# Optimization experiments

Measured on AMD Instinct MI355X. Metric: run time of the kernel, lower is better.

## Reference

```python
import jax, jax.numpy as jnp
import numpy as np

N_NODES = 100000
N_EDGES = 3200000
N_GRAPHS = 256
DIMS = [11, 200, 200, 200, 200, 200]  # acfg_init_dims + cfg_filters
CONCAT = sum(DIMS[1:])  # 1000


def setup_inputs() -> dict:
    key = jax.random.key(0)
    ks = jax.random.split(key, 32)
    d = {}
    d["x"] = jax.random.normal(ks[0], (N_NODES, DIMS[0]), jnp.float32)
    d["edge_index"] = jax.random.randint(ks[1], (2, N_EDGES), 0, N_NODES)
    d["batch"] = jnp.sort(jax.random.randint(ks[2], (N_NODES,), 0, N_GRAPHS))
    ki = 3
    # SAGEConv params: lin_l (neighbors, with bias) + lin_r (root, no bias)
    for i in range(5):
        fi, fo = DIMS[i], DIMS[i + 1]
        s = 1.0 / np.sqrt(fi)
        d[f"Wl{i+1}"] = jax.random.uniform(ks[ki], (fo, fi), jnp.float32, -s, s); ki += 1
        d[f"bl{i+1}"] = jnp.zeros((fo,), jnp.float32)
        d[f"Wr{i+1}"] = jax.random.uniform(ks[ki], (fo, fi), jnp.float32, -s, s); ki += 1
    # projection head 1000 -> 500 -> 250 -> 1
    for j, (fi, fo) in enumerate([(CONCAT, CONCAT // 2), (CONCAT // 2, CONCAT // 4), (CONCAT // 4, 1)]):
        s = 1.0 / np.sqrt(fi)
        d[f"pw{j+1}"] = jax.random.uniform(ks[ki], (fo, fi), jnp.float32, -s, s); ki += 1
        d[f"pb{j+1}"] = jnp.zeros((fo,), jnp.float32)
    return d


def reference(x, edge_index, batch,
              Wl1, bl1, Wr1, Wl2, bl2, Wr2, Wl3, bl3, Wr3,
              Wl4, bl4, Wr4, Wl5, bl5, Wr5,
              pw1, pb1, pw2, pb2, pw3, pb3):
    src, dst = edge_index[0], edge_index[1]
    # in-degree for mean aggregation (computed once, reused by all layers)
    deg = jax.ops.segment_sum(jnp.ones((src.shape[0],), x.dtype), dst, N_NODES)
    inv_deg = (1.0 / jnp.maximum(deg, 1.0))[:, None]

    def sage(h, Wl, bl, Wr):
        agg = jax.ops.segment_sum(h[src], dst, N_NODES) * inv_deg  # mean of neighbor feats
        return agg @ Wl.T + bl + h @ Wr.T

    layers = [(Wl1, bl1, Wr1), (Wl2, bl2, Wr2), (Wl3, bl3, Wr3), (Wl4, bl4, Wr4), (Wl5, bl5, Wr5)]
    h = x
    outs = []
    for Wl, bl, Wr in layers:
        h = jax.nn.relu(sage(h, Wl, bl, Wr))
        outs.append(h)
    hc = jnp.concatenate(outs, axis=1)  # [N, 1000]

    # global_mean_pool over graph ids
    cnt = jax.ops.segment_sum(jnp.ones((x.shape[0],), x.dtype), batch, N_GRAPHS)
    g = jax.ops.segment_sum(hc, batch, N_GRAPHS) / jnp.maximum(cnt, 1.0)[:, None]

    # dropout is identity in eval mode (functional.dropout with training=False)
    g = g @ pw1.T + pb1
    g = g @ pw2.T + pb2
    g = g @ pw3.T + pb3  # [num_graphs, 1]
    return jax.nn.sigmoid(g).squeeze(1)
```

## Files before the change

### kernel.cpp

```cpp
#include <hip/hip_runtime.h>
#include <math.h>

typedef __attribute__((ext_vector_type(4))) float floatx4;
typedef __attribute__((ext_vector_type(2))) float floatx2;

#define ROWP 256
#define R4   16
#define NT 14
#define NTC 13
#define KS 7
#define PACK_BYTES (NT*KS*64*8)
#define PACK1_BYTES (NT*64*8)
#define STAGE_BYTES (NTC*KS*64*8)
#define BSHIFT 6
#define EPB 8192
#define MAXBUCK 1600
#define PT_STRIDE 208

__device__ __forceinline__ unsigned short f2bf(float f){
    union { float f; unsigned u; } v; v.f = f;
    unsigned r = v.u + 0x7FFF + ((v.u >> 16) & 1);
    return (unsigned short)(r >> 16);
}
__device__ __forceinline__ unsigned pk4_fp8(float a, float b, float c, float d){
    int w = __builtin_amdgcn_cvt_pk_fp8_f32(a, b, 0, false);
    w = __builtin_amdgcn_cvt_pk_fp8_f32(c, d, w, true);
    return (unsigned)w;
}
__device__ __forceinline__ unsigned char b1_fp8(float a){
    int w = __builtin_amdgcn_cvt_pk_fp8_f32(a, a, 0, false);
    return (unsigned char)(w & 0xFF);
}


__global__ __launch_bounds__(256) void k_bin_hist(
    const int* __restrict__ dst, int* __restrict__ hist, int E, int nbuck)
{
    __shared__ int lh[MAXBUCK];
    for (int i = threadIdx.x; i < nbuck; i += 256) lh[i] = 0;
    __syncthreads();
    int base = blockIdx.x * EPB;
    #pragma unroll
    for (int k = 0; k < EPB / 256; ++k){
        int e = base + k * 256 + threadIdx.x;
        if (e < E) atomicAdd(&lh[dst[e] >> BSHIFT], 1);
    }
    __syncthreads();
    for (int i = threadIdx.x; i < nbuck; i += 256)
        hist[(size_t)blockIdx.x * nbuck + i] = lh[i];
}

__global__ __launch_bounds__(256) void k_col_scan(
    int* __restrict__ hist, int* __restrict__ T, int nblk, int nbuck)
{
    __shared__ int part[4][64];
    int w = threadIdx.x >> 6, l = threadIdx.x & 63;
    int b = blockIdx.x * 64 + l;
    int chunk = (nblk + 3) >> 2;
    int j0 = w * chunk, j1 = j0 + chunk; if (j1 > nblk) j1 = nblk;
    int s = 0;
    if (b < nbuck)
        for (int j = j0; j < j1; ++j) s += hist[(size_t)j * nbuck + b];
    part[w][l] = s;
    __syncthreads();
    if (b < nbuck){
        int run = 0;
        for (int w2 = 0; w2 < w; ++w2) run += part[w2][l];
        for (int j = j0; j < j1; ++j){
            int v = hist[(size_t)j * nbuck + b];
            hist[(size_t)j * nbuck + b] = run;
            run += v;
        }
        if (w == 3) T[b] = part[0][l] + part[1][l] + part[2][l] + part[3][l];
    }
}

__global__ __launch_bounds__(256) void k_scan_t(
    const int* __restrict__ T, int* __restrict__ tbase, int nbuck,
    const int* __restrict__ batch, int* __restrict__ gstart, int N, int NG)
{
    __shared__ int ts[256];
    int t = threadIdx.x;
    int v[8]; int s = 0;
    int base = t * 8;
    #pragma unroll
    for (int k = 0; k < 8; ++k){
        int idx = base + k;
        v[k] = (idx < nbuck) ? T[idx] : 0;
        s += v[k];
    }
    ts[t] = s; __syncthreads();
    #pragma unroll
    for (int off = 1; off < 256; off <<= 1){
        int p = (t >= off) ? ts[t - off] : 0;
        __syncthreads();
        ts[t] += p;
        __syncthreads();
    }
    int run = ts[t] - s;
    #pragma unroll
    for (int k = 0; k < 8; ++k){
        int idx = base + k;
        if (idx < nbuck) tbase[idx] = run;
        run += v[k];
    }
    if (t == 255) tbase[nbuck] = ts[255];

    for (int g = t; g <= NG; g += 256){
        int lo = 0, hi = N;
        while (lo < hi){
            int mid = (lo + hi) >> 1;
            if (batch[mid] < g) lo = mid + 1; else hi = mid;
        }
        gstart[g] = lo;
    }
}

__global__ __launch_bounds__(256) void k_bin_scatter(
    const int* __restrict__ src, const int* __restrict__ dst,
    const int* __restrict__ off, const int* __restrict__ tbase,
    unsigned* __restrict__ pairs, int E, int nbuck)
{
    __shared__ int lbase[MAXBUCK];
    __shared__ int lc[MAXBUCK];
    for (int i = threadIdx.x; i < nbuck; i += 256){
        lbase[i] = off[(size_t)blockIdx.x * nbuck + i] + tbase[i];
        lc[i] = 0;
    }
    __syncthreads();
    int base = blockIdx.x * EPB;
    #pragma unroll
    for (int k = 0; k < EPB / 256; ++k){
        int e = base + k * 256 + threadIdx.x;
        if (e < E){
            int d = dst[e];
            int b = d >> BSHIFT;
            int r = atomicAdd(&lc[b], 1);
            pairs[lbase[b] + r] = ((unsigned)(d & 63) << 26) | (unsigned)src[e];
        }
    }
}

__global__ __launch_bounds__(256) void k_bucket_deg(
    const unsigned* __restrict__ pairs, const int* __restrict__ tbase,
    int* __restrict__ deg, float* __restrict__ inv_deg, int N)
{
    __shared__ int ld[64];
    int b = blockIdx.x;
    if (threadIdx.x < 64) ld[threadIdx.x] = 0;
    __syncthreads();
    int pb = tbase[b], pe = tbase[b + 1];
    for (int e = pb + threadIdx.x; e < pe; e += 256)
        atomicAdd(&ld[pairs[e] >> 26], 1);
    __syncthreads();
    if (threadIdx.x < 64){
        int node = (b << BSHIFT) + threadIdx.x;
        if (node < N){
            int d = ld[threadIdx.x];
            deg[node] = d;
            inv_deg[node] = 1.0f / fmaxf((float)d, 1.0f);
        }
    }
}

__global__ __launch_bounds__(256) void k_place(
    const unsigned* __restrict__ pairs, const int* __restrict__ tbase,
    const int* __restrict__ row_ptr, int* __restrict__ srcs, int N)
{
    __shared__ int lrp[64];
    __shared__ int lcur[64];
    int b = blockIdx.x;
    if (threadIdx.x < 64){
        int node = (b << BSHIFT) + threadIdx.x;
        lrp[threadIdx.x] = (node < N) ? row_ptr[node] : 0;
        lcur[threadIdx.x] = 0;
    }
    __syncthreads();
    int pb = tbase[b], pe = tbase[b + 1];
    for (int e = pb + threadIdx.x; e < pe; e += 256){
        unsigned pr = pairs[e];
        int li = pr >> 26;
        int r = atomicAdd(&lcur[li], 1);
        srcs[lrp[li] + r] = (int)(pr & 0x03FFFFFFu);
    }
}


__global__ void k_scan_sums(const int* __restrict__ deg, int* __restrict__ csum, int N){
    __shared__ int sd[256];
    int base = blockIdx.x * 1024;
    int s = 0;
    for (int i = threadIdx.x; i < 1024; i += 256){
        int idx = base + i;
        s += (idx < N) ? deg[idx] : 0;
    }
    sd[threadIdx.x] = s; __syncthreads();
    for (int off = 128; off > 0; off >>= 1){
        if (threadIdx.x < off) sd[threadIdx.x] += sd[threadIdx.x + off];
        __syncthreads();
    }
    if (threadIdx.x == 0) csum[blockIdx.x] = sd[0];
}

__global__ void k_scan_apply(const int* __restrict__ deg, const int* __restrict__ csum,
                             int* __restrict__ row_ptr, int N, int E, int nchunks){
    __shared__ int ts[256];
    __shared__ int base_s;
    int partial = 0;
    for (int j = threadIdx.x; j < nchunks; j += 256)
        if (j < (int)blockIdx.x) partial += csum[j];
    ts[threadIdx.x] = partial; __syncthreads();
    for (int off = 128; off > 0; off >>= 1){
        if (threadIdx.x < off) ts[threadIdx.x] += ts[threadIdx.x + off];
        __syncthreads();
    }
    if (threadIdx.x == 0) base_s = ts[0];
    __syncthreads();
    int blk_base = base_s;
    __syncthreads();

    int base = blockIdx.x * 1024 + threadIdx.x * 4;
    int v[4]; int s = 0;
    #pragma unroll
    for (int j = 0; j < 4; ++j){
        int idx = base + j;
        v[j] = (idx < N) ? deg[idx] : 0;
        s += v[j];
    }
    ts[threadIdx.x] = s; __syncthreads();
    #pragma unroll
    for (int off = 1; off < 256; off <<= 1){
        int t = (threadIdx.x >= off) ? ts[threadIdx.x - off] : 0;
        __syncthreads();
        ts[threadIdx.x] += t;
        __syncthreads();
    }
    int excl = ts[threadIdx.x] - s + blk_base;
    #pragma unroll
    for (int j = 0; j < 4; ++j){
        int idx = base + j;
        if (idx < N) row_ptr[idx] = excl;
        excl += v[j];
    }
    if (blockIdx.x == 0 && threadIdx.x == 0) row_ptr[N] = E;
}


__global__ void k_pack_w(const float* W0, const float* W1, const float* W2, const float* W3,
                         const float* W4, const float* W5, const float* W6, const float* W7,
                         unsigned char* __restrict__ out){
    const float* Ws[8] = {W0,W1,W2,W3,W4,W5,W6,W7};
    const float* W = Ws[blockIdx.z];
    int lane = threadIdx.x;
    int n  = blockIdx.x * 16 + (lane & 15);
    int k0 = blockIdx.y * 32 + (lane >> 4) * 8;
    float f[8];
    #pragma unroll
    for (int j = 0; j < 8; ++j){
        int k = k0 + j;
        f[j] = (n < 200 && k < 200) ? W[n * 200 + k] : 0.f;
    }
    uint2 u;
    u.x = pk4_fp8(f[0], f[1], f[2], f[3]);
    u.y = pk4_fp8(f[4], f[5], f[6], f[7]);
    size_t off = ((((size_t)blockIdx.z * NT + blockIdx.x) * KS + blockIdx.y) * 64 + lane) * 8;
    *reinterpret_cast<uint2*>(out + off) = u;
}

__global__ __launch_bounds__(256) void k_pack_misc(
    const float* __restrict__ x, unsigned short* __restrict__ xp,
    unsigned char* __restrict__ xa,
    const float* __restrict__ Wl1, const float* __restrict__ Wr1,
    unsigned char* __restrict__ w1pack,
    const float* b0, const float* b1, const float* b2, const float* b3, const float* b4,
    float* __restrict__ biasp, int N, int xblk)
{
    int bid = blockIdx.x;
    if (bid < xblk){
        int i = bid * 256 + threadIdx.x;
        int node = i >> 4, c = i & 15;
        if (node < N){
            float f = (c < 11) ? x[(size_t)node * 11 + c] : 0.f;
            xp[i] = f2bf(f);
            xa[(size_t)node * 32 + 16 + c] = b1_fp8(f);
        }
        return;
    }
    int j = bid - xblk;
    if (j < NT){
        if (threadIdx.x >= 64) return;
        int lane = threadIdx.x;
        int n  = j * 16 + (lane & 15);
        int k0 = (lane >> 4) * 8;
        float f[8];
        #pragma unroll
        for (int jj = 0; jj < 8; ++jj){
            int k = k0 + jj;
            float v = 0.f;
            if (n < 200){
                if (k < 11)                 v = Wl1[n * 11 + k];
                else if (k >= 16 && k < 27) v = Wr1[n * 11 + (k - 16)];
            }
            f[jj] = v;
        }
        uint2 u;
        u.x = pk4_fp8(f[0], f[1], f[2], f[3]);
        u.y = pk4_fp8(f[4], f[5], f[6], f[7]);
        size_t off = ((size_t)j * 64 + lane) * 8;
        *reinterpret_cast<uint2*>(w1pack + off) = u;
        return;
    }
    int l = j - NT;
    const float* bs[5] = {b0,b1,b2,b3,b4};
    int c = threadIdx.x;
    if (c < ROWP) biasp[l * ROWP + c] = (c < 200) ? bs[l][c] : 0.f;
}


__global__ __launch_bounds__(256) void k_agg11(
    const unsigned short* __restrict__ xp, const int* __restrict__ row_ptr,
    const int* __restrict__ srcs, const float* __restrict__ inv_deg,
    unsigned char* __restrict__ xa, int N)
{
    int half = threadIdx.x >> 5;
    int node = blockIdx.x * 8 + half;
    int l = threadIdx.x & 31;
    if (node >= N) return;
    int beg = row_ptr[node], end = row_ptr[node + 1];

    float acc[12];
    #pragma unroll
    for (int i = 0; i < 12; ++i) acc[i] = 0.f;

    const uint4* x4 = reinterpret_cast<const uint4*>(xp);
    const uint2* x2 = reinterpret_cast<const uint2*>(xp);
    for (int e = beg + l; e < end; e += 32){
        int sn = srcs[e];
        uint4 a = x4[(size_t)sn * 2];
        uint2 b = x2[(size_t)sn * 4 + 2];
        union { unsigned u; float f; } c;
        c.u = a.x << 16;         acc[0] += c.f;
        c.u = a.x & 0xffff0000u; acc[1] += c.f;
        c.u = a.y << 16;         acc[2] += c.f;
        c.u = a.y & 0xffff0000u; acc[3] += c.f;
        c.u = a.z << 16;         acc[4] += c.f;
        c.u = a.z & 0xffff0000u; acc[5] += c.f;
        c.u = a.w << 16;         acc[6] += c.f;
        c.u = a.w & 0xffff0000u; acc[7] += c.f;
        c.u = b.x << 16;         acc[8] += c.f;
        c.u = b.x & 0xffff0000u; acc[9] += c.f;
        c.u = b.y << 16;         acc[10] += c.f;
        c.u = b.y & 0xffff0000u; acc[11] += c.f;
    }

    #pragma unroll
    for (int i = 0; i < 11; ++i){
        acc[i] += __shfl_xor(acc[i], 1, 64);
        acc[i] += __shfl_xor(acc[i], 2, 64);
        acc[i] += __shfl_xor(acc[i], 4, 64);
        acc[i] += __shfl_xor(acc[i], 8, 64);
        acc[i] += __shfl_xor(acc[i], 16, 64);
    }

    if (l == 0){
        float id = inv_deg[node];
        float v[12];
        #pragma unroll
        for (int i = 0; i < 11; ++i) v[i] = acc[i] * id;
        v[11] = 0.f;
        uint4 o;
        o.x = pk4_fp8(v[0], v[1], v[2], v[3]);
        o.y = pk4_fp8(v[4], v[5], v[6], v[7]);
        o.z = pk4_fp8(v[8], v[9], v[10], v[11]);
        o.w = 0u;
        *reinterpret_cast<uint4*>(xa + (size_t)node * 32) = o;
    }
}


__device__ __forceinline__ void accum_fp8v(floatx2* a, uint4 u){
    a[0] += __builtin_amdgcn_cvt_pk_f32_fp8((int)u.x, false);
    a[1] += __builtin_amdgcn_cvt_pk_f32_fp8((int)u.x, true );
    a[2] += __builtin_amdgcn_cvt_pk_f32_fp8((int)u.y, false);
    a[3] += __builtin_amdgcn_cvt_pk_f32_fp8((int)u.y, true );
    a[4] += __builtin_amdgcn_cvt_pk_f32_fp8((int)u.z, false);
    a[5] += __builtin_amdgcn_cvt_pk_f32_fp8((int)u.z, true );
    a[6] += __builtin_amdgcn_cvt_pk_f32_fp8((int)u.w, false);
    a[7] += __builtin_amdgcn_cvt_pk_f32_fp8((int)u.w, true );
}

__global__ __launch_bounds__(256) void k_agg200(
    const unsigned char* __restrict__ h8, const int* __restrict__ row_ptr,
    const int* __restrict__ srcs, const float* __restrict__ inv_deg,
    unsigned char* __restrict__ agg, int N)
{
    int node = blockIdx.x * 4 + (threadIdx.x >> 6);
    int lane = threadIdx.x & 63;
    if (node >= N) return;
    int g = lane >> 4;
    int l = lane & 15;
    int beg = row_ptr[node], end = row_ptr[node + 1];
    int nb = end - beg;

    floatx2 acc[8];
    #pragma unroll
    for (int i = 0; i < 8; ++i) acc[i] = (floatx2){0.f, 0.f};

    const uint4* h4 = reinterpret_cast<const uint4*>(h8);

    for (int t = 0; t < nb; t += 64){
        int cnt = nb - t; if (cnt > 64) cnt = 64;
        int eidx = t + lane;
        int si = srcs[beg + (eidx < nb ? eidx : nb - 1)];
        int jmax = (cnt - g + 3) >> 2;

        int j = 0;
        for (; j + 4 <= jmax; j += 4){
            int b0 = g + 4 * j;
            int s0 = __shfl(si, b0,      64);
            int s1 = __shfl(si, b0 + 4,  64);
            int s2 = __shfl(si, b0 + 8,  64);
            int s3 = __shfl(si, b0 + 12, 64);
            uint4 u0 = h4[(size_t)s0 * R4 + l];
            uint4 u1 = h4[(size_t)s1 * R4 + l];
            uint4 u2 = h4[(size_t)s2 * R4 + l];
            uint4 u3 = h4[(size_t)s3 * R4 + l];
            accum_fp8v(acc, u0);
            accum_fp8v(acc, u1);
            accum_fp8v(acc, u2);
            accum_fp8v(acc, u3);
        }
        for (; j < jmax; ++j){
            int s0 = __shfl(si, g + 4 * j, 64);
            uint4 u0 = h4[(size_t)s0 * R4 + l];
            accum_fp8v(acc, u0);
        }
    }

    float af[16];
    #pragma unroll
    for (int i = 0; i < 8; ++i){ af[2*i] = acc[i][0]; af[2*i+1] = acc[i][1]; }
    #pragma unroll
    for (int i = 0; i < 16; ++i){
        af[i] += __shfl_xor(af[i], 32, 64);
        af[i] += __shfl_xor(af[i], 16, 64);
    }

    if (g == 0){
        float id = inv_deg[node];
        uint4 o;
        o.x = pk4_fp8(af[0] * id,  af[1] * id,  af[2] * id,  af[3] * id);
        o.y = pk4_fp8(af[4] * id,  af[5] * id,  af[6] * id,  af[7] * id);
        o.z = pk4_fp8(af[8] * id,  af[9] * id,  af[10] * id, af[11] * id);
        o.w = pk4_fp8(af[12] * id, af[13] * id, af[14] * id, af[15] * id);
        *reinterpret_cast<uint4*>(agg + (size_t)node * ROWP + l * 16) = o;
    }
}


__global__ __launch_bounds__(256) void k_layer1_mfma(
    const unsigned char* __restrict__ xa, const unsigned char* __restrict__ W1p,
    const float* __restrict__ biasp, const int* __restrict__ batch,
    float* __restrict__ gsum, unsigned char* __restrict__ outp, int M)
{
    __shared__ __align__(16) unsigned char ptile[64 * PT_STRIDE];
    __shared__ int lb[64];
    const int wave = threadIdx.x >> 6;
    const int lane = threadIdx.x & 63;
    const int n = lane & 15;
    const int q = lane >> 4;
    const int r0 = blockIdx.x * 64;
    const int nrows = (M - r0 < 64) ? (M - r0) : 64;
    int row = r0 + wave * 16 + n;
    int rowc = row < M ? row : (M - 1);

    if (threadIdx.x < 64 && threadIdx.x < nrows) lb[threadIdx.x] = batch[r0 + threadIdx.x];

    long a = *reinterpret_cast<const long*>(xa + (size_t)rowc * 32 + q * 8);

    floatx4 acc[NTC];
    #pragma unroll
    for (int nt = 0; nt < NTC; ++nt){
        long b = *reinterpret_cast<const long*>(W1p + ((size_t)nt * 64 + lane) * 8);
        acc[nt] = __builtin_amdgcn_mfma_f32_16x16x32_fp8_fp8(a, b, (floatx4){0.f,0.f,0.f,0.f}, 0, 0, 0);
    }

    {
        int lr0 = wave * 16 + q * 4;
        #pragma unroll
        for (int nt = 0; nt < NTC; ++nt){
            float bsv = biasp[nt * 16 + n];
            #pragma unroll
            for (int r = 0; r < 4; ++r){
                float v = fmaxf(acc[nt][r] + bsv, 0.f);
                ptile[(lr0 + r) * PT_STRIDE + nt * 16 + n] = b1_fp8(v);
            }
        }
    }
    __syncthreads();

    {
        const uint4* s4 = reinterpret_cast<const uint4*>(ptile);
        int tot = nrows * 13;
        for (int i = threadIdx.x; i < tot; i += 256){
            int r = i / 13, c = i - r * 13;
            *reinterpret_cast<uint4*>(outp + (size_t)(r0 + r) * ROWP + c * 16) = s4[i];
        }
    }

    if (threadIdx.x < 50){
        int t = threadIdx.x;
        const unsigned* pd = reinterpret_cast<const unsigned*>(ptile);
        float s0 = 0.f, s1 = 0.f, s2 = 0.f, s3 = 0.f;
        int cur = lb[0];
        for (int r = 0; r < nrows; ++r){
            int gg = lb[r];
            if (gg != cur){
                float* gp = &gsum[(size_t)cur * 1000 + t * 4];
                atomicAdd(gp + 0, s0); atomicAdd(gp + 1, s1);
                atomicAdd(gp + 2, s2); atomicAdd(gp + 3, s3);
                s0 = s1 = s2 = s3 = 0.f;
                cur = gg;
            }
            unsigned u = pd[r * 52 + t];
            floatx2 lo = __builtin_amdgcn_cvt_pk_f32_fp8((int)u, false);
            floatx2 hi = __builtin_amdgcn_cvt_pk_f32_fp8((int)u, true);
            s0 += lo[0]; s1 += lo[1]; s2 += hi[0]; s3 += hi[1];
        }
        float* gp = &gsum[(size_t)cur * 1000 + t * 4];
        atomicAdd(gp + 0, s0); atomicAdd(gp + 1, s1);
        atomicAdd(gp + 2, s2); atomicAdd(gp + 3, s3);
    }
}

__global__ __launch_bounds__(256) void k_sage_mfma(
    const unsigned char* __restrict__ Aagg, const unsigned char* __restrict__ Ah,
    const unsigned char* __restrict__ Wlp, const unsigned char* __restrict__ Wrp,
    const float* __restrict__ biasp, const int* __restrict__ batch,
    float* __restrict__ gsum, int col_off,
    unsigned char* __restrict__ outp, int M)
{
    __shared__ __align__(16) unsigned char lw[STAGE_BYTES];
    __shared__ int lb[64];
    const int wave = threadIdx.x >> 6;
    const int lane = threadIdx.x & 63;
    const int n = lane & 15;
    const int q = lane >> 4;
    const int r0 = blockIdx.x * 64;
    const int nrows = (M - r0 < 64) ? (M - r0) : 64;
    int row = r0 + wave * 16 + n;
    int rowc = row < M ? row : (M - 1);

    if (threadIdx.x < 64 && threadIdx.x < nrows) lb[threadIdx.x] = batch[r0 + threadIdx.x];

    floatx4 acc[NTC];
    #pragma unroll
    for (int nt = 0; nt < NTC; ++nt) acc[nt] = (floatx4){0.f, 0.f, 0.f, 0.f};

    const unsigned char* Wp[2] = {Wlp, Wrp};
    const unsigned char* Ap[2] = {Aagg, Ah};

    #pragma unroll
    for (int phase = 0; phase < 2; ++phase){
        if (phase) __syncthreads();

        const unsigned char* arow = Ap[phase] + (size_t)rowc * ROWP + q * 8;
        long a[KS];
        #pragma unroll
        for (int ks = 0; ks < 6; ++ks)
            a[ks] = *reinterpret_cast<const long*>(arow + ks * 32);
        a[6] = (q < 2) ? *reinterpret_cast<const long*>(arow + 192) : 0L;

        {
            const uint4* src4 = reinterpret_cast<const uint4*>(Wp[phase]);
            uint4* dst4 = reinterpret_cast<uint4*>(lw);
            for (int i = threadIdx.x; i < STAGE_BYTES / 16; i += 256)
                dst4[i] = src4[i];
        }
        __syncthreads();

        #pragma unroll
        for (int ks = 0; ks < KS; ++ks){
            #pragma unroll
            for (int nt = 0; nt < NTC; ++nt){
                long b = *reinterpret_cast<const long*>(&lw[((nt * KS + ks) * 64 + lane) * 8]);
                acc[nt] = __builtin_amdgcn_mfma_f32_16x16x32_fp8_fp8(a[ks], b, acc[nt], 0, 0, 0);
            }
        }
    }
    __syncthreads();

    unsigned char* ptile = lw;
    {
        int lr0 = wave * 16 + q * 4;
        #pragma unroll
        for (int nt = 0; nt < NTC; ++nt){
            float bsv = biasp[nt * 16 + n];
            #pragma unroll
            for (int r = 0; r < 4; ++r){
                float v = fmaxf(acc[nt][r] + bsv, 0.f);
                ptile[(lr0 + r) * PT_STRIDE + nt * 16 + n] = b1_fp8(v);
            }
        }
    }
    __syncthreads();

    {
        const uint4* s4 = reinterpret_cast<const uint4*>(ptile);
        int tot = nrows * 13;
        for (int i = threadIdx.x; i < tot; i += 256){
            int r = i / 13, c = i - r * 13;
            *reinterpret_cast<uint4*>(outp + (size_t)(r0 + r) * ROWP + c * 16) = s4[i];
        }
    }

    if (threadIdx.x < 50){
        int t = threadIdx.x;
        const unsigned* pd = reinterpret_cast<const unsigned*>(ptile);
        float s0 = 0.f, s1 = 0.f, s2 = 0.f, s3 = 0.f;
        int cur = lb[0];
        for (int r = 0; r < nrows; ++r){
            int gg = lb[r];
            if (gg != cur){
                float* gp = &gsum[(size_t)cur * 1000 + col_off + t * 4];
                atomicAdd(gp + 0, s0); atomicAdd(gp + 1, s1);
                atomicAdd(gp + 2, s2); atomicAdd(gp + 3, s3);
                s0 = s1 = s2 = s3 = 0.f;
                cur = gg;
            }
            unsigned u = pd[r * 52 + t];
            floatx2 lo = __builtin_amdgcn_cvt_pk_f32_fp8((int)u, false);
            floatx2 hi = __builtin_amdgcn_cvt_pk_f32_fp8((int)u, true);
            s0 += lo[0]; s1 += lo[1]; s2 += hi[0]; s3 += hi[1];
        }
        float* gp = &gsum[(size_t)cur * 1000 + col_off + t * 4];
        atomicAdd(gp + 0, s0); atomicAdd(gp + 1, s1);
        atomicAdd(gp + 2, s2); atomicAdd(gp + 3, s3);
    }
}


__global__ __launch_bounds__(256) void k_mlp_first(
    const float* __restrict__ gsum, const int* __restrict__ gstart,
    const float* __restrict__ W, const float* __restrict__ b,
    float* __restrict__ outp)
{
    __shared__ __align__(16) float row[1000];
    int g = blockIdx.x;
    int cnt = gstart[g+1] - gstart[g];
    float inv = 1.0f / fmaxf((float)cnt, 1.0f);
    for (int i = threadIdx.x; i < 1000; i += 256)
        row[i] = gsum[(size_t)g * 1000 + i] * inv;
    __syncthreads();
    for (int c = threadIdx.x; c < 500; c += 256){
        const float4* w4 = reinterpret_cast<const float4*>(W + (size_t)c * 1000);
        const float4* r4 = reinterpret_cast<const float4*>(row);
        float s = b[c];
        for (int k = 0; k < 250; ++k){
            float4 wv = w4[k]; float4 rv = r4[k];
            s = fmaf(wv.x, rv.x, s);
            s = fmaf(wv.y, rv.y, s);
            s = fmaf(wv.z, rv.z, s);
            s = fmaf(wv.w, rv.w, s);
        }
        outp[(size_t)g * 500 + c] = s;
    }
}

__global__ __launch_bounds__(256) void k_mlp23(
    const float* __restrict__ t1, const float* __restrict__ W2,
    const float* __restrict__ b2, const float* __restrict__ W3,
    const float* __restrict__ b3, float* __restrict__ outp)
{
    __shared__ __align__(16) float row[500];
    __shared__ float red[256];
    int g = blockIdx.x;
    for (int i = threadIdx.x; i < 500; i += 256) row[i] = t1[(size_t)g * 500 + i];
    __syncthreads();
    float prod = 0.f;
    int c = threadIdx.x;
    if (c < 250){
        const float4* w4 = reinterpret_cast<const float4*>(W2 + (size_t)c * 500);
        const float4* r4 = reinterpret_cast<const float4*>(row);
        float s = b2[c];
        for (int k = 0; k < 125; ++k){
            float4 wv = w4[k]; float4 rv = r4[k];
            s = fmaf(wv.x, rv.x, s);
            s = fmaf(wv.y, rv.y, s);
            s = fmaf(wv.z, rv.z, s);
            s = fmaf(wv.w, rv.w, s);
        }
        prod = s * W3[c];
    }
    red[threadIdx.x] = prod;
    __syncthreads();
    for (int off = 128; off > 0; off >>= 1){
        if (threadIdx.x < off) red[threadIdx.x] += red[threadIdx.x + off];
        __syncthreads();
    }
    if (threadIdx.x == 0)
        outp[g] = 1.0f / (1.0f + expf(-(red[0] + b3[0])));
}


extern "C" void kernel_launch(void* const* d_in, const int* in_sizes, int n_in,
                              void* d_out, int out_size, void* d_ws, size_t ws_size,
                              hipStream_t stream)
{
    const float* x    = (const float*)d_in[0];
    const int*   ei   = (const int*)d_in[1];
    const int*   batch= (const int*)d_in[2];
    const float* Wl[5]; const float* bl[5]; const float* Wr[5];
    for (int i = 0; i < 5; ++i){
        Wl[i] = (const float*)d_in[3 + 3*i];
        bl[i] = (const float*)d_in[4 + 3*i];
        Wr[i] = (const float*)d_in[5 + 3*i];
    }
    const float* pw1 = (const float*)d_in[18]; const float* pb1 = (const float*)d_in[19];
    const float* pw2 = (const float*)d_in[20]; const float* pb2 = (const float*)d_in[21];
    const float* pw3 = (const float*)d_in[22]; const float* pb3 = (const float*)d_in[23];
    float* out = (float*)d_out;

    const int N  = in_sizes[2];
    const int E  = in_sizes[1] / 2;
    const int NG = out_size;
    const int* esrc = ei;
    const int* edst = ei + E;
    const int nbuck = (N + 63) >> BSHIFT;
    const int nblk  = (E + EPB - 1) / EPB;

    char* p = (char*)d_ws;
    auto carve = [&](size_t bytes)->void* {
        void* r = (void*)p;
        p += (bytes + 255) & ~(size_t)255;
        return r;
    };
    int*   deg     = (int*)  carve((size_t)N * 4);
    int*   row_ptr = (int*)  carve(((size_t)N + 1) * 4);
    int*   csum    = (int*)  carve(4096);
    int*   hist    = (int*)  carve((size_t)nblk * nbuck * 4);
    int*   Tb      = (int*)  carve((size_t)nbuck * 4);
    int*   tbase   = (int*)  carve(((size_t)nbuck + 1) * 4);
    float* invdeg  = (float*)carve((size_t)N * 4);
    int*   gstart  = (int*)  carve(((size_t)NG + 1) * 4);
    int*   srcs    = (int*)  carve((size_t)E * 4);
    unsigned* pairs = (unsigned*)carve((size_t)E * 4);
    unsigned short* xp    = (unsigned short*)carve((size_t)N * 16 * 2);
    unsigned char*  xa    = (unsigned char*) carve((size_t)N * 32);
    unsigned char*  agg8  = (unsigned char*) carve((size_t)N * ROWP);
    unsigned char*  h8A   = (unsigned char*) carve((size_t)N * ROWP);
    unsigned char*  h8B   = (unsigned char*) carve((size_t)N * ROWP);
    unsigned char*  wpack = (unsigned char*) carve((size_t)8 * PACK_BYTES);
    unsigned char*  w1pack= (unsigned char*) carve((size_t)PACK1_BYTES);
    float* biasp   = (float*)carve((size_t)5 * ROWP * 4);
    float* gsum    = (float*)carve((size_t)NG * 1000 * 4);
    float* t1      = (float*)carve((size_t)NG * 500 * 4);

    hipMemsetAsync(gsum, 0, (size_t)NG * 1000 * 4, stream);
    hipMemsetAsync(h8A, 0, (size_t)N * ROWP, stream);
    hipMemsetAsync(h8B, 0, (size_t)N * ROWP, stream);

    int xblk = (N * 16 + 255) / 256;
    k_pack_w<<<dim3(NT, KS, 8), 64, 0, stream>>>(
        Wl[1], Wr[1], Wl[2], Wr[2], Wl[3], Wr[3], Wl[4], Wr[4], wpack);
    k_pack_misc<<<xblk + NT + 5, 256, 0, stream>>>(
        x, xp, xa, Wl[0], Wr[0], w1pack,
        bl[0], bl[1], bl[2], bl[3], bl[4], biasp, N, xblk);

    k_bin_hist<<<nblk, 256, 0, stream>>>(edst, hist, E, nbuck);
    k_col_scan<<<(nbuck + 63) / 64, 256, 0, stream>>>(hist, Tb, nblk, nbuck);
    k_scan_t<<<1, 256, 0, stream>>>(Tb, tbase, nbuck, batch, gstart, N, NG);
    k_bin_scatter<<<nblk, 256, 0, stream>>>(esrc, edst, hist, tbase, pairs, E, nbuck);
    k_bucket_deg<<<nbuck, 256, 0, stream>>>(pairs, tbase, deg, invdeg, N);
    int nchunks = (N + 1023) / 1024;
    k_scan_sums<<<nchunks, 256, 0, stream>>>(deg, csum, N);
    k_scan_apply<<<nchunks, 256, 0, stream>>>(deg, csum, row_ptr, N, E, nchunks);
    k_place<<<nbuck, 256, 0, stream>>>(pairs, tbase, row_ptr, srcs, N);

    int gb = (N + 63) / 64;
    k_agg11<<<(N + 7) / 8, 256, 0, stream>>>(xp, row_ptr, srcs, invdeg, xa, N);
    k_layer1_mfma<<<gb, 256, 0, stream>>>(xa, w1pack, biasp, batch, gsum, h8A, N);

    unsigned char* hc = h8A; unsigned char* hn = h8B;
    int ab = (N + 3) / 4;
    for (int L = 1; L < 5; ++L){
        k_agg200<<<ab, 256, 0, stream>>>(hc, row_ptr, srcs, invdeg, agg8, N);
        const unsigned char* Wlp = wpack + (size_t)((L-1)*2 + 0) * PACK_BYTES;
        const unsigned char* Wrp = wpack + (size_t)((L-1)*2 + 1) * PACK_BYTES;
        k_sage_mfma<<<gb, 256, 0, stream>>>(agg8, hc, Wlp, Wrp,
                                            biasp + L * ROWP, batch, gsum, 200 * L,
                                            hn, N);
        unsigned char* t = hc; hc = hn; hn = t;
    }

    k_mlp_first<<<NG, 256, 0, stream>>>(gsum, gstart, pw1, pb1, t1);
    k_mlp23<<<NG, 256, 0, stream>>>(t1, pw2, pb2, pw3, pb3, out);
}
```

Before: 1.082 ms.

## Fuse bucket degree, row-pointer scan and placement into one kernel

Replaces the four-kernel CSR build (bucket degree, two-pass global scan, placement) with a single per-bucket kernel. It derives row_ptr locally from the bucket base offset plus a serial 64-entry prefix sum, and caches the bucket's pairs in LDS so they are read from global memory once. It also doubles edges per block in the binning kernels, which halves the histogram size and the number of blocks. This removes three launches and the global deg array, but adds a 16KB LDS buffer per block that may lower occupancy.

```diff
diff --git a/kernel.cpp b/kernel.cpp
--- a/kernel.cpp
+++ b/kernel.cpp
@@ -13,9 +13,10 @@
 #define PACK1_BYTES (NT*64*8)
 #define STAGE_BYTES (NTC*KS*64*8)
 #define BSHIFT 6
-#define EPB 8192
+#define EPB 16384
 #define MAXBUCK 1600
 #define PT_STRIDE 208
+#define PAIR_LDS 4096
 
 __device__ __forceinline__ unsigned short f2bf(float f){
     union { float f; unsigned u; } v; v.f = f;
@@ -141,108 +142,51 @@
     }
 }
 
-__global__ __launch_bounds__(256) void k_bucket_deg(
+__global__ __launch_bounds__(256) void k_bucket_build(
     const unsigned* __restrict__ pairs, const int* __restrict__ tbase,
-    int* __restrict__ deg, float* __restrict__ inv_deg, int N)
+    float* __restrict__ inv_deg, int* __restrict__ row_ptr,
+    int* __restrict__ srcs, int N, int E, int nbuck)
 {
     __shared__ int ld[64];
+    __shared__ int lrp[64];
+    __shared__ int lcur[64];
+    __shared__ unsigned lpr[PAIR_LDS];
     int b = blockIdx.x;
-    if (threadIdx.x < 64) ld[threadIdx.x] = 0;
+    if (threadIdx.x < 64){ ld[threadIdx.x] = 0; lcur[threadIdx.x] = 0; }
     __syncthreads();
     int pb = tbase[b], pe = tbase[b + 1];
-    for (int e = pb + threadIdx.x; e < pe; e += 256)
-        atomicAdd(&ld[pairs[e] >> 26], 1);
-    __syncthreads();
+    int ne = pe - pb;
+    const bool inLds = (ne <= PAIR_LDS);
+
+    for (int e = pb + threadIdx.x; e < pe; e += 256){
+        unsigned pr = pairs[e];
+        if (inLds) lpr[e - pb] = pr;
+        atomicAdd(&ld[pr >> 26], 1);
+    }
+    __syncthreads();
+
+    if (threadIdx.x == 0){
+        int run = pb;
+        #pragma unroll
+        for (int i = 0; i < 64; ++i){ lrp[i] = run; run += ld[i]; }
+    }
+    __syncthreads();
+
     if (threadIdx.x < 64){
         int node = (b << BSHIFT) + threadIdx.x;
         if (node < N){
-            int d = ld[threadIdx.x];
-            deg[node] = d;
-            inv_deg[node] = 1.0f / fmaxf((float)d, 1.0f);
-        }
-    }
-}
-
-__global__ __launch_bounds__(256) void k_place(
-    const unsigned* __restrict__ pairs, const int* __restrict__ tbase,
-    const int* __restrict__ row_ptr, int* __restrict__ srcs, int N)
-{
-    __shared__ int lrp[64];
-    __shared__ int lcur[64];
-    int b = blockIdx.x;
-    if (threadIdx.x < 64){
-        int node = (b << BSHIFT) + threadIdx.x;
-        lrp[threadIdx.x] = (node < N) ? row_ptr[node] : 0;
-        lcur[threadIdx.x] = 0;
-    }
-    __syncthreads();
-    int pb = tbase[b], pe = tbase[b + 1];
+            inv_deg[node] = 1.0f / fmaxf((float)ld[threadIdx.x], 1.0f);
+            row_ptr[node] = lrp[threadIdx.x];
+        }
+    }
+    if (b == nbuck - 1 && threadIdx.x == 0) row_ptr[N] = E;
+
     for (int e = pb + threadIdx.x; e < pe; e += 256){
-        unsigned pr = pairs[e];
+        unsigned pr = inLds ? lpr[e - pb] : pairs[e];
         int li = pr >> 26;
         int r = atomicAdd(&lcur[li], 1);
         srcs[lrp[li] + r] = (int)(pr & 0x03FFFFFFu);
     }
-}
-
-
-__global__ void k_scan_sums(const int* __restrict__ deg, int* __restrict__ csum, int N){
-    __shared__ int sd[256];
-    int base = blockIdx.x * 1024;
-    int s = 0;
-    for (int i = threadIdx.x; i < 1024; i += 256){
-        int idx = base + i;
-        s += (idx < N) ? deg[idx] : 0;
-    }
-    sd[threadIdx.x] = s; __syncthreads();
-    for (int off = 128; off > 0; off >>= 1){
-        if (threadIdx.x < off) sd[threadIdx.x] += sd[threadIdx.x + off];
-        __syncthreads();
-    }
-    if (threadIdx.x == 0) csum[blockIdx.x] = sd[0];
-}
-
-__global__ void k_scan_apply(const int* __restrict__ deg, const int* __restrict__ csum,
-                             int* __restrict__ row_ptr, int N, int E, int nchunks){
-    __shared__ int ts[256];
-    __shared__ int base_s;
-    int partial = 0;
-    for (int j = threadIdx.x; j < nchunks; j += 256)
-        if (j < (int)blockIdx.x) partial += csum[j];
-    ts[threadIdx.x] = partial; __syncthreads();
-    for (int off = 128; off > 0; off >>= 1){
-        if (threadIdx.x < off) ts[threadIdx.x] += ts[threadIdx.x + off];
-        __syncthreads();
-    }
-    if (threadIdx.x == 0) base_s = ts[0];
-    __syncthreads();
-    int blk_base = base_s;
-    __syncthreads();
-
-    int base = blockIdx.x * 1024 + threadIdx.x * 4;
-    int v[4]; int s = 0;
-    #pragma unroll
-    for (int j = 0; j < 4; ++j){
-        int idx = base + j;
-        v[j] = (idx < N) ? deg[idx] : 0;
-        s += v[j];
-    }
-    ts[threadIdx.x] = s; __syncthreads();
-    #pragma unroll
-    for (int off = 1; off < 256; off <<= 1){
-        int t = (threadIdx.x >= off) ? ts[threadIdx.x - off] : 0;
-        __syncthreads();
-        ts[threadIdx.x] += t;
-        __syncthreads();
-    }
-    int excl = ts[threadIdx.x] - s + blk_base;
-    #pragma unroll
-    for (int j = 0; j < 4; ++j){
-        int idx = base + j;
-        if (idx < N) row_ptr[idx] = excl;
-        excl += v[j];
-    }
-    if (blockIdx.x == 0 && threadIdx.x == 0) row_ptr[N] = E;
 }
 
 
@@ -735,9 +679,7 @@
         p += (bytes + 255) & ~(size_t)255;
         return r;
     };
-    int*   deg     = (int*)  carve((size_t)N * 4);
     int*   row_ptr = (int*)  carve(((size_t)N + 1) * 4);
-    int*   csum    = (int*)  carve(4096);
     int*   hist    = (int*)  carve((size_t)nblk * nbuck * 4);
     int*   Tb      = (int*)  carve((size_t)nbuck * 4);
     int*   tbase   = (int*)  carve(((size_t)nbuck + 1) * 4);
@@ -771,11 +713,7 @@
     k_col_scan<<<(nbuck + 63) / 64, 256, 0, stream>>>(hist, Tb, nblk, nbuck);
     k_scan_t<<<1, 256, 0, stream>>>(Tb, tbase, nbuck, batch, gstart, N, NG);
     k_bin_scatter<<<nblk, 256, 0, stream>>>(esrc, edst, hist, tbase, pairs, E, nbuck);
-    k_bucket_deg<<<nbuck, 256, 0, stream>>>(pairs, tbase, deg, invdeg, N);
-    int nchunks = (N + 1023) / 1024;
-    k_scan_sums<<<nchunks, 256, 0, stream>>>(deg, csum, N);
-    k_scan_apply<<<nchunks, 256, 0, stream>>>(deg, csum, row_ptr, N, E, nchunks);
-    k_place<<<nbuck, 256, 0, stream>>>(pairs, tbase, row_ptr, srcs, N);
+    k_bucket_build<<<nbuck, 256, 0, stream>>>(pairs, tbase, invdeg, row_ptr, srcs, N, E, nbuck);
 
     int gb = (N + 63) / 64;
     k_agg11<<<(N + 7) / 8, 256, 0, stream>>>(xp, row_ptr, srcs, invdeg, xa, N);
```

Measured after the change: 1.091 ms. About the same (+0.8%).
